# Optimization experiments

Hardware: AMD Instinct MI355X
Metric: run time of the kernel (lower is better)

The kernel has to match this reference:

```python
import jax, jax.numpy as jnp
import numpy as np

DIM = 1024
HEADS = 16
DIM_HEAD = 64
INNER = HEADS * DIM_HEAD  # 1024
B, N = 4, 1024
SCALE = DIM_HEAD ** -0.5


def _layernorm(t, g, b, eps=1e-5):
    mu = jnp.mean(t, axis=-1, keepdims=True)
    var = jnp.var(t, axis=-1, keepdims=True)
    return (t - mu) * jax.lax.rsqrt(var + eps) * g + b


def setup_inputs() -> dict:
    key = jax.random.key(0)
    ks = jax.random.split(key, 8)
    return {
        "x": jax.random.normal(ks[0], (B, N, DIM), dtype=jnp.float32),
        "y": jax.random.normal(ks[1], (B, N, DIM), dtype=jnp.float32),
        "gx": jnp.ones((DIM,), jnp.float32),
        "bx": jnp.zeros((DIM,), jnp.float32),
        "gy": jnp.ones((DIM,), jnp.float32),
        "by": jnp.zeros((DIM,), jnp.float32),
        "Wqkv_x": jax.random.normal(ks[2], (DIM, 3 * INNER), jnp.float32) * 0.02,
        "Wqkv_y": jax.random.normal(ks[3], (DIM, 3 * INNER), jnp.float32) * 0.02,
        "Wout_x": jax.random.normal(ks[4], (INNER, DIM), jnp.float32) * 0.02,
        "bout_x": jnp.zeros((DIM,), jnp.float32),
        "Wout_y": jax.random.normal(ks[5], (INNER, DIM), jnp.float32) * 0.02,
        "bout_y": jnp.zeros((DIM,), jnp.float32),
    }


def _split_heads(t):
    b, n, _ = t.shape
    return t.reshape(b, n, HEADS, DIM_HEAD).transpose(0, 2, 1, 3)  # b h n d


def reference(x, y, gx, bx, gy, by, Wqkv_x, Wqkv_y, Wout_x, bout_x, Wout_y, bout_y):
    xn = _layernorm(x, gx, bx)
    yn = _layernorm(y, gy, by)
    qx, kx, vx = [_split_heads(t) for t in jnp.split(xn @ Wqkv_x, 3, axis=-1)]
    qy, ky, vy = [_split_heads(t) for t in jnp.split(yn @ Wqkv_y, 3, axis=-1)]
    # concat along HEADS dim -> 2h heads; each stream's heads attend within that stream
    q = jnp.concatenate([qx, qy], axis=1)
    k = jnp.concatenate([kx, ky], axis=1)
    v = jnp.concatenate([vx, vy], axis=1)
    dots = jnp.einsum('bhid,bhjd->bhij', q, k) * SCALE  # [B, 2h, N, N]
    attn = jax.nn.softmax(dots, axis=-1)
    out = jnp.einsum('bhij,bhjd->bhid', attn, v)  # [B, 2h, N, d]
    xo = out[:, :HEADS]  # original code uses the x-chunk for BOTH outputs (faithful)
    xo = xo.transpose(0, 2, 1, 3).reshape(xo.shape[0], xo.shape[2], INNER)  # b n (h d)
    out_x = xo @ Wout_x + bout_x
    out_y = xo @ Wout_y + bout_y
    return (out_x, out_y)
```

## Files before the change

### kernel.cpp

```cpp
#include <hip/hip_runtime.h>

typedef __attribute__((ext_vector_type(8))) short s16x8;
typedef __attribute__((ext_vector_type(4))) float f32x4;
typedef unsigned short u16;

#define DEV __device__ __forceinline__

DEV u16 f2bf(float f) {
    unsigned u = __builtin_bit_cast(unsigned, f);
    unsigned r = u + 0x7fffu + ((u >> 16) & 1u);
    return (u16)(r >> 16);
}

DEV float exp2a(float x) {
    float r;
    asm("v_exp_f32 %0, %1" : "=v"(r) : "v"(x));
    return r;
}

DEV unsigned cvtpk(float lo, float hi) {
    unsigned r;
    asm("v_cvt_pk_bf16_f32 %0, %1, %2" : "=v"(r) : "v"(lo), "v"(hi));
    return r;
}

DEV void gload_lds16(const void* g, void* l) {
    __builtin_amdgcn_global_load_lds(
        (const __attribute__((address_space(1))) unsigned int*)g,
        (__attribute__((address_space(3))) unsigned int*)l, 16, 0, 0);
}

DEV f32x4 mfma16(s16x8 a, s16x8 b, f32x4 c) {
    return __builtin_amdgcn_mfma_f32_16x16x32_bf16(a, b, c, 0, 0, 0);
}

__global__ __launch_bounds__(256) void ln_kernel(const float* __restrict__ x,
                                                 const float* __restrict__ g,
                                                 const float* __restrict__ b,
                                                 u16* __restrict__ xn) {
    const int row = blockIdx.x, t = threadIdx.x;
    const float4 v = *(const float4*)(x + (size_t)row * 1024 + t * 4);
    float s1 = v.x + v.y + v.z + v.w;
    float s2 = v.x * v.x + v.y * v.y + v.z * v.z + v.w * v.w;
#pragma unroll
    for (int d = 1; d < 64; d <<= 1) {
        s1 += __shfl_xor(s1, d);
        s2 += __shfl_xor(s2, d);
    }
    __shared__ float red[8];
    if ((t & 63) == 0) { red[(t >> 6) * 2] = s1; red[(t >> 6) * 2 + 1] = s2; }
    __syncthreads();
    s1 = red[0] + red[2] + red[4] + red[6];
    s2 = red[1] + red[3] + red[5] + red[7];
    const float mu = s1 * (1.0f / 1024.0f);
    const float var = s2 * (1.0f / 1024.0f) - mu * mu;
    const float rs = rsqrtf(var + 1e-5f);
    const float4 gv = *(const float4*)(g + t * 4);
    const float4 bv = *(const float4*)(b + t * 4);
    ushort4 o;
    o.x = f2bf((v.x - mu) * rs * gv.x + bv.x);
    o.y = f2bf((v.y - mu) * rs * gv.y + bv.y);
    o.z = f2bf((v.z - mu) * rs * gv.z + bv.z);
    o.w = f2bf((v.w - mu) * rs * gv.w + bv.w);
    *(ushort4*)(xn + (size_t)row * 1024 + t * 4) = o;
}

__global__ __launch_bounds__(256) void transpose_w(const float* __restrict__ src,
                                                   u16* __restrict__ dst, int ld) {
    __shared__ float tile[64][68];
    const int t = threadIdx.x;
    const int n0 = blockIdx.x * 64, k0 = blockIdx.y * 64;
    const int kl = t >> 4, nl = (t & 15) * 4;
#pragma unroll
    for (int p = 0; p < 4; ++p) {
        float4 v = *(const float4*)(src + (size_t)(k0 + kl + p * 16) * ld + n0 + nl);
        tile[kl + p * 16][nl + 0] = v.x;
        tile[kl + p * 16][nl + 1] = v.y;
        tile[kl + p * 16][nl + 2] = v.z;
        tile[kl + p * 16][nl + 3] = v.w;
    }
    __syncthreads();
    const int nl2 = t >> 2, kc = (t & 3) * 16;
    __align__(16) u16 tmp[16];
#pragma unroll
    for (int j = 0; j < 16; ++j) tmp[j] = f2bf(tile[kc + j][nl2]);
    u16* d = dst + (size_t)(n0 + nl2) * 1024 + k0 + kc;
    ((uint4*)d)[0] = ((const uint4*)tmp)[0];
    ((uint4*)d)[1] = ((const uint4*)tmp)[1];
}

__global__ __launch_bounds__(256) void transpose_v(const u16* __restrict__ V,
                                                   u16* __restrict__ Vt) {
    __shared__ u16 tile[64][72];
    const int t = threadIdx.x;
    const int j0 = blockIdx.x * 64;
    const int bh = blockIdx.y;
    const u16* src = V + (size_t)bh * 65536;
    const int jl = t >> 4, dl = (t & 15) * 4;
#pragma unroll
    for (int p = 0; p < 4; ++p) {
        ushort4 v = *(const ushort4*)(src + (size_t)(j0 + jl + p * 16) * 64 + dl);
        *(ushort4*)&tile[jl + p * 16][dl] = v;
    }
    __syncthreads();
    const int dl2 = t >> 2, jc = (t & 3) * 16;
    __align__(16) u16 tmp[16];
#pragma unroll
    for (int j = 0; j < 16; ++j) tmp[j] = tile[jc + j][dl2];
    u16* d = Vt + (size_t)bh * 65536 + (size_t)dl2 * 1024 + j0 + jc;
    ((uint4*)d)[0] = ((const uint4*)tmp)[0];
    ((uint4*)d)[1] = ((const uint4*)tmp)[1];
}

template <int EPI>
__global__ __launch_bounds__(256) void gemm_bt(const u16* __restrict__ A,
                                               const u16* __restrict__ B,
                                               u16* __restrict__ Qb, u16* __restrict__ Kb,
                                               u16* __restrict__ Vb,
                                               const float* __restrict__ bx,
                                               const float* __restrict__ by,
                                               float* __restrict__ out, int K) {
    __shared__ __align__(16) u16 As[2][128 * 32];
    __shared__ __align__(16) u16 Bs[2][128 * 32];
    const int tid = threadIdx.x, lane = tid & 63;
    const int wave = tid >> 6, wm = wave >> 1, wn = wave & 1;
    const int m0 = blockIdx.y * 128, n0 = blockIdx.x * 128;
    const int lr = lane & 15, cg = lane >> 4;
    f32x4 acc[4][4] = {};

#define STAGE(bufi, k0)                                                            \
    do {                                                                           \
        _Pragma("unroll") for (int i = 0; i < 2; ++i) {                            \
            int idx = i * 256 + tid;                                               \
            int row = idx >> 2, p = idx & 3;                                       \
            int kk = (k0) + ((p ^ ((row >> 1) & 3)) << 3);                         \
            gload_lds16(A + (size_t)(m0 + row) * K + kk, &As[bufi][idx * 8]);      \
            gload_lds16(B + (size_t)(n0 + row) * K + kk, &Bs[bufi][idx * 8]);      \
        }                                                                          \
    } while (0)

    STAGE(0, 0);
    asm volatile("s_waitcnt vmcnt(0)" ::: "memory");
    __syncthreads();
    const int nk = K >> 5;
    for (int t = 0; t < nk; ++t) {
        const int buf = t & 1;
        if (t + 1 < nk) STAGE(buf ^ 1, (t + 1) << 5);
        s16x8 a[4], b[4];
#pragma unroll
        for (int f = 0; f < 4; ++f) {
            int r = wm * 64 + f * 16 + lr;
            a[f] = *(const s16x8*)&As[buf][r * 32 + ((cg ^ ((r >> 1) & 3)) << 3)];
            int r2 = wn * 64 + f * 16 + lr;
            b[f] = *(const s16x8*)&Bs[buf][r2 * 32 + ((cg ^ ((r2 >> 1) & 3)) << 3)];
        }
#pragma unroll
        for (int fm = 0; fm < 4; ++fm)
#pragma unroll
            for (int fn = 0; fn < 4; ++fn) acc[fm][fn] = mfma16(a[fm], b[fn], acc[fm][fn]);
        asm volatile("s_waitcnt vmcnt(0)" ::: "memory");
        __syncthreads();
    }
#undef STAGE

    const int colb = n0 + wn * 64 + lr;
    const int rowb = m0 + wm * 64 + cg * 4;
    if (EPI == 0) {
#pragma unroll
        for (int fn = 0; fn < 4; ++fn) {
            const int col = colb + fn * 16;
            const int which = col >> 10, hd = col & 1023;
            const int h = hd >> 6, dd = hd & 63;
            u16* dst = (which == 0) ? Qb : (which == 1) ? Kb : Vb;
            const float sc = (which == 0) ? 0.18033688011112042f : 1.0f;
#pragma unroll
            for (int fm = 0; fm < 4; ++fm)
#pragma unroll
                for (int r = 0; r < 4; ++r) {
                    const int tk = rowb + fm * 16 + r;
                    const int bb = tk >> 10, ii = tk & 1023;
                    dst[(size_t)(((bb << 4) + h) * 1024 + ii) * 64 + dd] =
                        f2bf(acc[fm][fn][r] * sc);
                }
        }
    } else {
#pragma unroll
        for (int fn = 0; fn < 4; ++fn) {
            const int col = colb + fn * 16;
            float bias;
            float* ob;
            if (col < 1024) { bias = bx[col]; ob = out + col; }
            else { bias = by[col - 1024]; ob = out + 4194304 + (col - 1024); }
#pragma unroll
            for (int fm = 0; fm < 4; ++fm)
#pragma unroll
                for (int r = 0; r < 4; ++r) {
                    const int tk = rowb + fm * 16 + r;
                    ob[(size_t)tk * 1024] = acc[fm][fn][r] + bias;
                }
        }
    }
}

__global__ __launch_bounds__(256) void attn_kernel(const u16* __restrict__ Q,
                                                   const u16* __restrict__ Kg,
                                                   const u16* __restrict__ Vt,
                                                   u16* __restrict__ xo) {
    __shared__ __align__(16) u16 Ks[2][64 * 64];
    __shared__ __align__(16) u16 Vs[2][64 * 64];
    __shared__ __align__(16) u16 Ps[4][32 * 64];
    const int tid = threadIdx.x, lane = tid & 63, w = tid >> 6;
    const int bh = blockIdx.x >> 3, qblk = blockIdx.x & 7;
    const u16* Qh = Q + (size_t)bh * 65536;
    const u16* Kh = Kg + (size_t)bh * 65536;
    const u16* Vh = Vt + (size_t)bh * 65536;
    const int lr = lane & 15, cg = lane >> 4;
    const int q0 = qblk * 128 + w * 32;
    u16* Pw = &Ps[w][0];

    s16x8 qf[2][2];
#pragma unroll
    for (int qg = 0; qg < 2; ++qg)
#pragma unroll
        for (int ks = 0; ks < 2; ++ks)
            qf[qg][ks] =
                *(const s16x8*)(Qh + (size_t)(q0 + qg * 16 + lr) * 64 + ks * 32 + cg * 8);

    f32x4 o[2][4] = {};
    float l_s[2] = {0.f, 0.f};
    float m_s[2] = {-3e38f, -3e38f};
    int ba[4];
#pragma unroll
    for (int r = 0; r < 4; ++r) ba[r] = (cg * 4 + r) * 4;

#define STAGEKV(bufi, kv0)                                                               \
    do {                                                                                 \
        _Pragma("unroll") for (int i = 0; i < 2; ++i) {                                  \
            int idx = i * 256 + tid;                                                     \
            int row = idx >> 3, p = idx & 7;                                             \
            gload_lds16(Kh + (size_t)((kv0) + row) * 64 + ((p ^ (row & 7)) << 3),        \
                        &Ks[bufi][idx * 8]);                                             \
            gload_lds16(Vh + (size_t)row * 1024 + (kv0) + ((p ^ (row & 7)) << 3),        \
                        &Vs[bufi][idx * 8]);                                             \
        }                                                                                \
    } while (0)

    STAGEKV(0, 0);
    asm volatile("s_waitcnt vmcnt(0)" ::: "memory");
    __syncthreads();

    for (int t = 0; t < 16; ++t) {
        const int buf = t & 1;
        if (t < 15) STAGEKV(buf ^ 1, (t + 1) * 64);

        f32x4 s[2][4] = {};
#pragma unroll
        for (int fn = 0; fn < 4; ++fn) {
            const int r = fn * 16 + lr;
#pragma unroll
            for (int ks = 0; ks < 2; ++ks) {
                const int c = cg + ks * 4;
                s16x8 kf = *(const s16x8*)&Ks[buf][r * 64 + ((c ^ (r & 7)) << 3)];
                s[0][fn] = mfma16(kf, qf[0][ks], s[0][fn]);
                s[1][fn] = mfma16(kf, qf[1][ks], s[1][fn]);
            }
        }

#pragma unroll
        for (int qg = 0; qg < 2; ++qg) {
            float tm = -3e38f;
#pragma unroll
            for (int fn = 0; fn < 4; ++fn)
#pragma unroll
                for (int r = 0; r < 4; ++r) tm = fmaxf(tm, s[qg][fn][r]);
            tm = fmaxf(tm, __shfl_xor(tm, 16));
            tm = fmaxf(tm, __shfl_xor(tm, 32));
            if (!__all(tm <= m_s[qg] + 8.0f)) {
                const float mn = fmaxf(m_s[qg], tm);
                const float corr = exp2a(m_s[qg] - mn);
                m_s[qg] = mn;
                l_s[qg] *= corr;
                f32x4 corr_o;
#pragma unroll
                for (int r = 0; r < 4; ++r)
                    corr_o[r] = __builtin_bit_cast(
                        float,
                        __builtin_amdgcn_ds_bpermute(ba[r], __builtin_bit_cast(int, corr)));
#pragma unroll
                for (int fd = 0; fd < 4; ++fd) o[qg][fd] *= corr_o;
            }
            const float mn = m_s[qg];
            float rs = 0.f;
            const int prow = (qg * 16 + lr) * 64;
#pragma unroll
            for (int fn = 0; fn < 4; ++fn) {
                const float p0 = exp2a(s[qg][fn][0] - mn);
                const float p1 = exp2a(s[qg][fn][1] - mn);
                const float p2 = exp2a(s[qg][fn][2] - mn);
                const float p3 = exp2a(s[qg][fn][3] - mn);
                rs += (p0 + p1) + (p2 + p3);
                uint2 dd;
                dd.x = cvtpk(p0, p1);
                dd.y = cvtpk(p2, p3);
                *(uint2*)(Pw + prow + (((2 * fn + (cg >> 1)) ^ (lr & 7)) << 3) +
                          ((cg & 1) << 2)) = dd;
            }
            rs += __shfl_xor(rs, 16);
            rs += __shfl_xor(rs, 32);
            l_s[qg] += rs;
        }

        s16x8 pf[2][2];
#pragma unroll
        for (int qg = 0; qg < 2; ++qg)
#pragma unroll
            for (int ks = 0; ks < 2; ++ks)
                pf[qg][ks] = *(const s16x8*)(Pw + (qg * 16 + lr) * 64 +
                                             (((4 * ks + cg) ^ (lr & 7)) << 3));
#pragma unroll
        for (int fd = 0; fd < 4; ++fd) {
            const int rr = fd * 16 + lr;
#pragma unroll
            for (int ks = 0; ks < 2; ++ks) {
                const int c = cg + ks * 4;
                s16x8 vf = *(const s16x8*)&Vs[buf][rr * 64 + ((c ^ (rr & 7)) << 3)];
                o[0][fd] = mfma16(pf[0][ks], vf, o[0][fd]);
                o[1][fd] = mfma16(pf[1][ks], vf, o[1][fd]);
            }
        }
        asm volatile("s_waitcnt vmcnt(0)" ::: "memory");
        __syncthreads();
    }
#undef STAGEKV

    const int b = bh >> 4, h = bh & 15;
#pragma unroll
    for (int qg = 0; qg < 2; ++qg) {
        f32x4 inv;
#pragma unroll
        for (int r = 0; r < 4; ++r) {
            const float lq = __builtin_bit_cast(
                float, __builtin_amdgcn_ds_bpermute(ba[r], __builtin_bit_cast(int, l_s[qg])));
            inv[r] = 1.0f / lq;
        }
#pragma unroll
        for (int r = 0; r < 4; ++r) {
            const int qrow = q0 + qg * 16 + cg * 4 + r;
#pragma unroll
            for (int fd = 0; fd < 4; ++fd)
                xo[(size_t)(b * 1024 + qrow) * 1024 + h * 64 + fd * 16 + lr] =
                    f2bf(o[qg][fd][r] * inv[r]);
        }
    }
}

extern "C" void kernel_launch(void* const* d_in, const int* in_sizes, int n_in,
                              void* d_out, int out_size, void* d_ws, size_t ws_size,
                              hipStream_t stream) {
    const float* x = (const float*)d_in[0];
    const float* gx = (const float*)d_in[2];
    const float* bxv = (const float*)d_in[3];
    const float* Wqkv = (const float*)d_in[6];
    const float* Woutx = (const float*)d_in[8];
    const float* boutx = (const float*)d_in[9];
    const float* Wouty = (const float*)d_in[10];
    const float* bouty = (const float*)d_in[11];
    float* out = (float*)d_out;

    u16* ws = (u16*)d_ws;
    u16* xn = ws;
    u16* wqkv_t = xn + 4096 * 1024;
    u16* wout_t = wqkv_t + 3072 * 1024;
    u16* Qb = wout_t + 2048 * 1024;
    u16* Kb = Qb + 64 * 1024 * 64;
    u16* Vb = Kb + 64 * 1024 * 64;
    u16* Vtb = Vb + 64 * 1024 * 64;
    u16* xob = Vtb + 64 * 1024 * 64;

    ln_kernel<<<4096, 256, 0, stream>>>(x, gx, bxv, xn);
    transpose_w<<<dim3(48, 16), 256, 0, stream>>>(Wqkv, wqkv_t, 3072);
    transpose_w<<<dim3(16, 16), 256, 0, stream>>>(Woutx, wout_t, 1024);
    transpose_w<<<dim3(16, 16), 256, 0, stream>>>(Wouty, wout_t + 1024 * 1024, 1024);
    gemm_bt<0><<<dim3(24, 32), 256, 0, stream>>>(xn, wqkv_t, Qb, Kb, Vb, nullptr,
                                                 nullptr, nullptr, 1024);
    transpose_v<<<dim3(16, 64), 256, 0, stream>>>(Vb, Vtb);
    attn_kernel<<<512, 256, 0, stream>>>(Qb, Kb, Vtb, xob);
    gemm_bt<1><<<dim3(16, 32), 256, 0, stream>>>(xob, wout_t, nullptr, nullptr, nullptr,
                                                 boutx, bouty, out, 1024);
}
```

Before: 122.3 us.

## Replace GEMMs with 8-wave 256-row tiled kernel using quarter-tile pipelined phases

```diff
diff --git a/kernel.cpp b/kernel.cpp
--- a/kernel.cpp
+++ b/kernel.cpp
@@ -32,6 +32,11 @@
 
 DEV f32x4 mfma16(s16x8 a, s16x8 b, f32x4 c) {
     return __builtin_amdgcn_mfma_f32_16x16x32_bf16(a, b, c, 0, 0, 0);
+}
+
+template <int N>
+DEV void vmwait() {
+    asm volatile("s_waitcnt vmcnt(%0)" ::"n"(N) : "memory");
 }
 
 __global__ __launch_bounds__(256) void ln_kernel(const float* __restrict__ x,
@@ -112,92 +117,162 @@
     ((uint4*)d)[1] = ((const uint4*)tmp)[1];
 }
 
-template <int EPI>
-__global__ __launch_bounds__(256) void gemm_bt(const u16* __restrict__ A,
-                                               const u16* __restrict__ B,
-                                               u16* __restrict__ Qb, u16* __restrict__ Kb,
-                                               u16* __restrict__ Vb,
-                                               const float* __restrict__ bx,
-                                               const float* __restrict__ by,
-                                               float* __restrict__ out, int K) {
-    __shared__ __align__(16) u16 As[2][128 * 32];
-    __shared__ __align__(16) u16 Bs[2][128 * 32];
+template <int BN, int WM, int EPI>
+__global__ __launch_bounds__(512, 2) void gemm8(const u16* __restrict__ A,
+                                                const u16* __restrict__ B,
+                                                u16* __restrict__ Qb, u16* __restrict__ Kb,
+                                                u16* __restrict__ Vb,
+                                                const float* __restrict__ bx,
+                                                const float* __restrict__ by,
+                                                float* __restrict__ out, int NBX) {
+    constexpr int BM = 256, WN = 8 / WM;
+    constexpr int TM = BM / WM, TN = BN / WN;
+    constexpr int MQ = TM / 32, NQ = TN / 32;
+    constexpr int HA = TM / 2, HB = TN / 2;
+    constexpr int CHA = 1024;
+    constexpr int CHB = BN * 4;
+    constexpr int GA = 2, GB = CHB / 512;
+    constexpr int NI = 8;
+
+    __shared__ __align__(16) u16 As[2 * 2 * CHA * 8];
+    __shared__ __align__(16) u16 Bs[2 * 2 * CHB * 8];
+
     const int tid = threadIdx.x, lane = tid & 63;
-    const int wave = tid >> 6, wm = wave >> 1, wn = wave & 1;
-    const int m0 = blockIdx.y * 128, n0 = blockIdx.x * 128;
+    const int wave = tid >> 6;
+    const int wm = wave / WN, wn = wave % WN;
     const int lr = lane & 15, cg = lane >> 4;
-    f32x4 acc[4][4] = {};
-
-#define STAGE(bufi, k0)                                                            \
-    do {                                                                           \
-        _Pragma("unroll") for (int i = 0; i < 2; ++i) {                            \
-            int idx = i * 256 + tid;                                               \
-            int row = idx >> 2, p = idx & 3;                                       \
-            int kk = (k0) + ((p ^ ((row >> 1) & 3)) << 3);                         \
-            gload_lds16(A + (size_t)(m0 + row) * K + kk, &As[bufi][idx * 8]);      \
-            gload_lds16(B + (size_t)(n0 + row) * K + kk, &Bs[bufi][idx * 8]);      \
-        }                                                                          \
+
+    const int nwg = NBX * 16;
+    const int bid = blockIdx.x;
+    const int bid2 = (bid & 7) * (nwg >> 3) + (bid >> 3);
+    const int bxi = bid2 % NBX, byi = bid2 / NBX;
+    const int m0 = byi * 256, n0 = bxi * BN;
+
+    const u16* __restrict__ Ag = A + (size_t)m0 * 1024;
+    const u16* __restrict__ Bg = B + (size_t)n0 * 1024;
+
+    f32x4 acc[2 * MQ][2 * NQ] = {};
+
+#define STG_A(b, h, t)                                                              \
+    do {                                                                            \
+        _Pragma("unroll") for (int u = 0; u < GA; ++u) {                            \
+            const int idx = u * 512 + tid;                                          \
+            const int loc = idx >> 3, pp = idx & 7;                                 \
+            const int row = (loc & (HA - 1)) | ((h)*HA) | ((loc / HA) * 2 * HA);    \
+            gload_lds16(Ag + (size_t)row * 1024 + (t)*64 + ((pp ^ (row & 7)) << 3), \
+                        &As[(((b)*2 + (h)) * CHA + idx) * 8]);                      \
+        }                                                                           \
     } while (0)
-
-    STAGE(0, 0);
-    asm volatile("s_waitcnt vmcnt(0)" ::: "memory");
-    __syncthreads();
-    const int nk = K >> 5;
-    for (int t = 0; t < nk; ++t) {
-        const int buf = t & 1;
-        if (t + 1 < nk) STAGE(buf ^ 1, (t + 1) << 5);
-        s16x8 a[4], b[4];
-#pragma unroll
-        for (int f = 0; f < 4; ++f) {
-            int r = wm * 64 + f * 16 + lr;
-            a[f] = *(const s16x8*)&As[buf][r * 32 + ((cg ^ ((r >> 1) & 3)) << 3)];
-            int r2 = wn * 64 + f * 16 + lr;
-            b[f] = *(const s16x8*)&Bs[buf][r2 * 32 + ((cg ^ ((r2 >> 1) & 3)) << 3)];
-        }
-#pragma unroll
-        for (int fm = 0; fm < 4; ++fm)
-#pragma unroll
-            for (int fn = 0; fn < 4; ++fn) acc[fm][fn] = mfma16(a[fm], b[fn], acc[fm][fn]);
-        asm volatile("s_waitcnt vmcnt(0)" ::: "memory");
-        __syncthreads();
-    }
-#undef STAGE
-
-    const int colb = n0 + wn * 64 + lr;
-    const int rowb = m0 + wm * 64 + cg * 4;
-    if (EPI == 0) {
-#pragma unroll
-        for (int fn = 0; fn < 4; ++fn) {
-            const int col = colb + fn * 16;
-            const int which = col >> 10, hd = col & 1023;
-            const int h = hd >> 6, dd = hd & 63;
-            u16* dst = (which == 0) ? Qb : (which == 1) ? Kb : Vb;
-            const float sc = (which == 0) ? 0.18033688011112042f : 1.0f;
-#pragma unroll
-            for (int fm = 0; fm < 4; ++fm)
+#define STG_B(b, h, t)                                                              \
+    do {                                                                            \
+        _Pragma("unroll") for (int u = 0; u < GB; ++u) {                            \
+            const int idx = u * 512 + tid;                                          \
+            const int loc = idx >> 3, pp = idx & 7;                                 \
+            const int row = (loc & (HB - 1)) | ((h)*HB) | ((loc / HB) * 2 * HB);    \
+            gload_lds16(Bg + (size_t)row * 1024 + (t)*64 + ((pp ^ (row & 7)) << 3), \
+                        &Bs[(((b)*2 + (h)) * CHB + idx) * 8]);                      \
+        }                                                                           \
+    } while (0)
+
+#define READS(bb, lm, ln)                                                           \
+    s16x8 af[MQ][2], bf[NQ][2];                                                     \
+    _Pragma("unroll") for (int mf = 0; mf < MQ; ++mf)                               \
+        _Pragma("unroll") for (int ks = 0; ks < 2; ++ks)                            \
+            af[mf][ks] = *(const s16x8*)&As[((((bb)*2 + (lm)) * CHA) +              \
+                                             (mf * 16 + lr + wm * HA) * 8 +         \
+                                             ((cg + ks * 4) ^ (lr & 7))) * 8];      \
+    _Pragma("unroll") for (int nf = 0; nf < NQ; ++nf)                               \
+        _Pragma("unroll") for (int ks = 0; ks < 2; ++ks)                            \
+            bf[nf][ks] = *(const s16x8*)&Bs[((((bb)*2 + (ln)) * CHB) +              \
+                                             (nf * 16 + lr + wn * HB) * 8 +         \
+                                             ((cg + ks * 4) ^ (lr & 7))) * 8];
+
+#define MM(lm, ln)                                                                  \
+    __builtin_amdgcn_s_setprio(1);                                                  \
+    _Pragma("unroll") for (int mf = 0; mf < MQ; ++mf)                               \
+        _Pragma("unroll") for (int nf = 0; nf < NQ; ++nf)                           \
+            _Pragma("unroll") for (int ks = 0; ks < 2; ++ks)                        \
+                acc[(lm)*MQ + mf][(ln)*NQ + nf] = mfma16(                           \
+                    af[mf][ks], bf[nf][ks], acc[(lm)*MQ + mf][(ln)*NQ + nf]);       \
+    __builtin_amdgcn_s_setprio(0);
+
+#define BAR() asm volatile("s_barrier" ::: "memory")
+
+#define PHASE(bb, lm, ln, STAGE_STMT, WAIT_STMT)                                    \
+    {                                                                               \
+        READS(bb, lm, ln);                                                          \
+        STAGE_STMT;                                                                 \
+        WAIT_STMT;                                                                  \
+        BAR();                                                                      \
+        MM(lm, ln);                                                                 \
+    }
+
+    STG_A(0, 0, 0);
+    STG_A(0, 1, 0);
+    STG_B(0, 0, 0);
+    STG_B(0, 1, 0);
+    STG_A(1, 0, 1);
+    STG_B(1, 0, 1);
+    vmwait<GA + GB>();
+    BAR();
+
+#pragma unroll 1
+    for (int i = 0; i < NI - 1; ++i) {
+        const int t1 = 2 * i + 1, t2 = 2 * i + 2, t3 = 2 * i + 3;
+        PHASE(0, 0, 0, STG_A(1, 1, t1), (void)0);
+        PHASE(0, 0, 1, STG_B(1, 1, t1), (void)0);
+        PHASE(0, 1, 0, STG_A(0, 0, t2), (void)0);
+        PHASE(0, 1, 1, STG_B(0, 0, t2), vmwait<GA + GB>());
+        PHASE(1, 0, 0, STG_A(0, 1, t2), (void)0);
+        PHASE(1, 0, 1, STG_B(0, 1, t2), (void)0);
+        PHASE(1, 1, 0, STG_A(1, 0, t3), (void)0);
+        PHASE(1, 1, 1, STG_B(1, 0, t3), vmwait<GA + GB>());
+    }
+    PHASE(0, 0, 0, STG_A(1, 1, 15), (void)0);
+    PHASE(0, 0, 1, STG_B(1, 1, 15), (void)0);
+    PHASE(0, 1, 0, (void)0, (void)0);
+    PHASE(0, 1, 1, (void)0, vmwait<0>());
+    { READS(1, 0, 0); MM(0, 0); }
+    { READS(1, 0, 1); MM(0, 1); }
+    { READS(1, 1, 0); MM(1, 0); }
+    { READS(1, 1, 1); MM(1, 1); }
+
+#undef STG_A
+#undef STG_B
+#undef READS
+#undef MM
+#undef BAR
+#undef PHASE
+
+#pragma unroll
+    for (int am = 0; am < 2 * MQ; ++am) {
+        const int lm = am / MQ, mf = am % MQ;
+        const int rowb = m0 + wm * TM + lm * HA + mf * 16 + cg * 4;
+#pragma unroll
+        for (int an = 0; an < 2 * NQ; ++an) {
+            const int ln = an / NQ, nf = an % NQ;
+            const int col = n0 + wn * TN + ln * HB + nf * 16 + lr;
+            if (EPI == 0) {
+                const int which = col >> 10, hd = col & 1023;
+                const int h = hd >> 6, dd = hd & 63;
+                u16* dst = (which == 0) ? Qb : (which == 1) ? Kb : Vb;
+                const float sc = (which == 0) ? 0.18033688011112042f : 1.0f;
 #pragma unroll
                 for (int r = 0; r < 4; ++r) {
-                    const int tk = rowb + fm * 16 + r;
-                    const int bb = tk >> 10, ii = tk & 1023;
-                    dst[(size_t)(((bb << 4) + h) * 1024 + ii) * 64 + dd] =
-                        f2bf(acc[fm][fn][r] * sc);
+                    const int tk = rowb + r;
+                    const int bb2 = tk >> 10, ii = tk & 1023;
+                    dst[(size_t)(((bb2 << 4) + h) * 1024 + ii) * 64 + dd] =
+                        f2bf(acc[am][an][r] * sc);
                 }
-        }
-    } else {
-#pragma unroll
-        for (int fn = 0; fn < 4; ++fn) {
-            const int col = colb + fn * 16;
-            float bias;
-            float* ob;
-            if (col < 1024) { bias = bx[col]; ob = out + col; }
-            else { bias = by[col - 1024]; ob = out + 4194304 + (col - 1024); }
-#pragma unroll
-            for (int fm = 0; fm < 4; ++fm)
-#pragma unroll
-                for (int r = 0; r < 4; ++r) {
-                    const int tk = rowb + fm * 16 + r;
-                    ob[(size_t)tk * 1024] = acc[fm][fn][r] + bias;
-                }
+            } else {
+                float bias;
+                float* ob;
+                if (col < 1024) { bias = bx[col]; ob = out + col; }
+                else { bias = by[col - 1024]; ob = out + 4194304 + (col - 1024); }
+#pragma unroll
+                for (int r = 0; r < 4; ++r)
+                    ob[(size_t)(rowb + r) * 1024] = acc[am][an][r] + bias;
+            }
         }
     }
 }
@@ -381,10 +456,10 @@
     transpose_w<<<dim3(48, 16), 256, 0, stream>>>(Wqkv, wqkv_t, 3072);
     transpose_w<<<dim3(16, 16), 256, 0, stream>>>(Woutx, wout_t, 1024);
     transpose_w<<<dim3(16, 16), 256, 0, stream>>>(Wouty, wout_t + 1024 * 1024, 1024);
-    gemm_bt<0><<<dim3(24, 32), 256, 0, stream>>>(xn, wqkv_t, Qb, Kb, Vb, nullptr,
-                                                 nullptr, nullptr, 1024);
+    gemm8<256, 2, 0><<<192, 512, 0, stream>>>(xn, wqkv_t, Qb, Kb, Vb, nullptr, nullptr,
+                                              nullptr, 12);
     transpose_v<<<dim3(16, 64), 256, 0, stream>>>(Vb, Vtb);
     attn_kernel<<<512, 256, 0, stream>>>(Qb, Kb, Vtb, xob);
-    gemm_bt<1><<<dim3(16, 32), 256, 0, stream>>>(xob, wout_t, nullptr, nullptr, nullptr,
-                                                 boutx, bouty, out, 1024);
-}
+    gemm8<128, 4, 1><<<256, 512, 0, stream>>>(xob, wout_t, nullptr, nullptr, nullptr,
+                                              boutx, bouty, out, 16);
+}
```

After: 126.8 us. 1.04x slower.
